# Kernel optimization log

Measured on AMD Instinct MI355X. Metric: run time of the kernel, lower is better.

The kernel has to match this reference:

```python
import jax, jax.numpy as jnp
import numpy as np

DIM = 768
NUM_HEADS = 12
HEAD_DIM = DIM // NUM_HEADS
SCALE = HEAD_DIM ** -0.5
B, N = 8, 1024


def setup_inputs() -> dict:
    key = jax.random.key(0)
    k1, k2, k3, k4, k5 = jax.random.split(key, 5)
    x = jax.random.normal(k1, (B, N, DIM), dtype=jnp.float32)
    # qkv: Linear(dim, 3*dim, bias=False); proj: Linear(dim, dim) with bias
    w_qkv = jax.random.normal(k2, (3 * DIM, DIM), dtype=jnp.float32) * (DIM ** -0.5)
    w_proj = jax.random.normal(k3, (DIM, DIM), dtype=jnp.float32) * (DIM ** -0.5)
    b_proj = jnp.zeros((DIM,), dtype=jnp.float32)
    # learned attention mask parameter, shape (H, L, L) with L >= N
    att_mask = jax.random.normal(k4, (NUM_HEADS, N, N), dtype=jnp.float32)
    return {"x": x, "w_qkv": w_qkv, "w_proj": w_proj, "b_proj": b_proj, "att_mask": att_mask}


def reference(x, w_qkv, w_proj, b_proj, att_mask):
    Bx, Nx, C = x.shape
    # qkv projection -> (3, B, H, N, head_dim)
    qkv = (x @ w_qkv.T).reshape(Bx, Nx, 3, NUM_HEADS, C // NUM_HEADS)
    qkv = jnp.transpose(qkv, (2, 0, 3, 1, 4))
    q, k, v = qkv[0], qkv[1], qkv[2]  # gpd_ratio==active_ratio==1 -> scaling factor 1
    # scores [B, H, N, N]
    attn = jnp.einsum('bhnd,bhmd->bhnm', q, k) * SCALE
    # custom sigmoid mask gating before softmax (broadcast over batch)
    attn = attn * jax.nn.sigmoid(att_mask[:, :Nx, :Nx])[None, :, :, :]
    attn = jax.nn.softmax(attn, axis=-1)
    out = jnp.einsum('bhnm,bhmd->bhnd', attn, v)
    out = jnp.transpose(out, (0, 2, 1, 3)).reshape(Bx, Nx, C)
    return out @ w_proj.T + b_proj
```

## Files before the change

kernel.cpp:

```cpp
#include <hip/hip_runtime.h>
#include <math.h>
#include <stdint.h>

typedef unsigned short u16;
typedef __attribute__((ext_vector_type(8))) short short8;
typedef __attribute__((ext_vector_type(4))) float f32x4;

#define GATE_SCALE 0.18033688011112042f

#if __has_builtin(__builtin_amdgcn_exp2f)
#define FEXP2(x) __builtin_amdgcn_exp2f(x)
#else
#define FEXP2(x) exp2f(x)
#endif

__device__ __forceinline__ u16 f2b(float f) {
    union { float f; unsigned u; } v; v.f = f;
    unsigned r = v.u + 0x7fffu + ((v.u >> 16) & 1u);
    return (u16)(r >> 16);
}
__device__ __forceinline__ u16 f2b_hu(float f) {
    union { float f; unsigned u; } v; v.f = f;
    return (u16)((v.u + 0x8000u) >> 16);
}
__device__ __forceinline__ float b2f(u16 u) {
    union { float f; unsigned u; } v; v.u = ((unsigned)u) << 16; return v.f;
}

#define GLL16(gsrc, ldsbase) __builtin_amdgcn_global_load_lds(                    \
    (__attribute__((address_space(1))) void*)(uintptr_t)(gsrc),                   \
    (__attribute__((address_space(3))) void*)(uint32_t)(uintptr_t)(ldsbase),      \
    16, 0, 0)

#define NX4  1572864
#define NW14 442368
#define NW24 147456
#define NXW4 (NX4 + NW14 + NW24)

__global__ __launch_bounds__(256) void prep_xw(
    const float4* __restrict__ x, const float4* __restrict__ wq,
    const float4* __restrict__ wp,
    ushort4* __restrict__ xb, ushort4* __restrict__ wqb,
    ushort4* __restrict__ wpb)
{
    size_t i = (size_t)blockIdx.x * 256 + threadIdx.x;
    float4 v; ushort4* dst; size_t j;
    if (i < NX4)            { j = i;               v = x[j];  dst = xb;  }
    else if (i < NX4 + NW14){ j = i - NX4;         v = wq[j]; dst = wqb; }
    else                    { j = i - (NX4 + NW14);v = wp[j]; dst = wpb; }
    ushort4 o; o.x = f2b(v.x); o.y = f2b(v.y); o.z = f2b(v.z); o.w = f2b(v.w);
    dst[j] = o;
}

__global__ __launch_bounds__(256) void prep_gate(
    const float4* __restrict__ mask4, u16* __restrict__ gp)
{
    __shared__ u16 L[64][72];
    const int bid = blockIdx.x;
    const int kt = bid & 15, qt = (bid >> 4) & 15, h = bid >> 8;
    const int t = threadIdx.x;

    #pragma unroll
    for (int s = 0; s < 4; ++s) {
        const int idx = t + s * 256;
        const int row = idx >> 4, c4 = idx & 15;
        float4 v = mask4[(size_t)(h * 1024 + qt * 64 + row) * 256 + kt * 16 + c4];
        L[row][c4 * 4 + 0] = f2b(GATE_SCALE / (1.f + __expf(-v.x)));
        L[row][c4 * 4 + 1] = f2b(GATE_SCALE / (1.f + __expf(-v.y)));
        L[row][c4 * 4 + 2] = f2b(GATE_SCALE / (1.f + __expf(-v.z)));
        L[row][c4 * 4 + 3] = f2b(GATE_SCALE / (1.f + __expf(-v.w)));
    }
    __syncthreads();

    const int w = t >> 6, l = t & 63;
    const int fq = l >> 4, fr = l & 15;
    union { u16 u[16]; float4 f[2]; } vals;
    #pragma unroll
    for (int i = 0; i < 4; ++i)
        #pragma unroll
        for (int nt = 0; nt < 4; ++nt)
            vals.u[i * 4 + nt] = L[16 * w + 4 * fq + i][nt * 16 + fr];
    float4* dst = (float4*)(gp + (size_t)bid * 4096 + (size_t)t * 16);
    dst[0] = vals.f[0];
    dst[1] = vals.f[1];
}

__global__ __launch_bounds__(256) void qkv_gemm(
    const u16* __restrict__ xb, const u16* __restrict__ wb,
    u16* __restrict__ qb, u16* __restrict__ kb, u16* __restrict__ vb)
{
    __shared__ u16 As[2][4096];
    __shared__ u16 Bs[2][4096];
    const int t = threadIdx.x, l = t & 63, w = t >> 6;
    const int wm = (w & 1) * 64, wn = (w >> 1) * 64;
    const int m0 = blockIdx.y * 128, c0 = blockIdx.x * 128;

    f32x4 acc[4][4];
    #pragma unroll
    for (int i = 0; i < 4; ++i)
        #pragma unroll
        for (int j = 0; j < 4; ++j) { f32x4 z = {0.f,0.f,0.f,0.f}; acc[i][j] = z; }

    const int srow = l >> 2, sseg = l & 3;
    const int gcol = ((sseg ^ (srow & 3)) << 3);
    const u16* a0 = xb + (size_t)(m0 + w * 16 + srow) * 768 + gcol;
    const u16* a1 = a0 + (size_t)64 * 768;
    const u16* b0p = wb + (size_t)(c0 + w * 16 + srow) * 768 + gcol;
    const u16* b1p = b0p + (size_t)64 * 768;
    const int wofs = w * 512;

    const int fr = l & 15, fq = l >> 4;
    const int fseg = (fq ^ (fr & 3)) << 3;

    GLL16(a0, &As[0][wofs]);
    GLL16(a1, &As[0][2048 + wofs]);
    GLL16(b0p, &Bs[0][wofs]);
    GLL16(b1p, &Bs[0][2048 + wofs]);

    for (int kt = 0; kt < 24; ++kt) {
        __syncthreads();
        if (kt < 23) {
            const int kn = (kt + 1) * 32;
            const int nb = (kt + 1) & 1;
            GLL16(a0 + kn, &As[nb][wofs]);
            GLL16(a1 + kn, &As[nb][2048 + wofs]);
            GLL16(b0p + kn, &Bs[nb][wofs]);
            GLL16(b1p + kn, &Bs[nb][2048 + wofs]);
        }
        const u16* A = As[kt & 1];
        const u16* B = Bs[kt & 1];
        short8 af[4], bf[4];
        #pragma unroll
        for (int mt = 0; mt < 4; ++mt)
            af[mt] = *(const short8*)&A[(wm + mt * 16 + fr) * 32 + fseg];
        #pragma unroll
        for (int nt = 0; nt < 4; ++nt)
            bf[nt] = *(const short8*)&B[(wn + nt * 16 + fr) * 32 + fseg];
        #pragma unroll
        for (int mt = 0; mt < 4; ++mt)
            #pragma unroll
            for (int nt = 0; nt < 4; ++nt)
                acc[mt][nt] = __builtin_amdgcn_mfma_f32_16x16x32_bf16(
                    af[mt], bf[nt], acc[mt][nt], 0, 0, 0);
    }

    const int b = m0 >> 10;
    const int n0 = m0 & 1023;
    #pragma unroll
    for (int nt = 0; nt < 4; ++nt) {
        const int c = c0 + wn + nt * 16 + fr;
        const int which = c / 768;
        const int rem = c - which * 768;
        const int h = rem >> 6, d = rem & 63;
        if (which < 2) {
            u16* dst = ((which == 0) ? qb : kb)
                       + ((size_t)(b * 12 + h) * 1024) * 64 + d;
            #pragma unroll
            for (int mt = 0; mt < 4; ++mt)
                #pragma unroll
                for (int r = 0; r < 4; ++r) {
                    const int n = n0 + wm + mt * 16 + fq * 4 + r;
                    dst[(size_t)n * 64] = f2b(acc[mt][nt][r]);
                }
        } else {
            u16* dst = vb + ((size_t)(b * 12 + h) * 64 + d) * 1024
                          + n0 + wm + fq * 4;
            #pragma unroll
            for (int mt = 0; mt < 4; ++mt) {
                ushort4 pk;
                pk.x = f2b(acc[mt][nt][0]); pk.y = f2b(acc[mt][nt][1]);
                pk.z = f2b(acc[mt][nt][2]); pk.w = f2b(acc[mt][nt][3]);
                *(ushort4*)(dst + mt * 16) = pk;
            }
        }
    }
}

__global__ __launch_bounds__(256, 3) void flash_attn(
    const u16* __restrict__ qb, const u16* __restrict__ kb,
    const u16* __restrict__ vt, const u16* __restrict__ gperm,
    u16* __restrict__ aob)
{
    __shared__ u16 Qs[8192], Ks[4096], Vts[4096], Ps[4096];
    const int t = threadIdx.x, l = t & 63, w = t >> 6;
    const int bid = blockIdx.x;
    const int qtb = bid & 7, bh = bid >> 3;
    const int h = bh % 12, b = bh / 12;
    const int q0 = qtb * 128;

    const u16* hq = qb + (size_t)bh * 65536;
    const u16* hk = kb + (size_t)bh * 65536;
    const u16* hv = vt + (size_t)bh * 65536;
    const u16* hgb = gperm + ((size_t)h * 256 + qtb * 32) * 4096 + (w * 64 + l) * 16;

    const int sr = l >> 3, ss = l & 7;
    const int sg = ((ss ^ (sr & 7)) << 3);
    const int j0 = w * 2, j1 = j0 + 1;

    #pragma unroll
    for (int jq = 0; jq < 4; ++jq) {
        const int j = w * 4 + jq;
        GLL16(hq + (size_t)(q0 + j * 8 + sr) * 64 + sg, Qs + j * 512);
    }
    GLL16(hk + (size_t)(j0 * 8 + sr) * 64 + sg, Ks + j0 * 512);
    GLL16(hk + (size_t)(j1 * 8 + sr) * 64 + sg, Ks + j1 * 512);
    GLL16(hv + (size_t)(j0 * 8 + sr) * 1024 + sg, Vts + j0 * 512);
    GLL16(hv + (size_t)(j1 * 8 + sr) * 1024 + sg, Vts + j1 * 512);
    __syncthreads();

    const int fq = l >> 4, fr = l & 15;
    const int sega = ((fq ^ (fr & 7)) << 3);
    const int segb = (((4 + fq) ^ (fr & 7)) << 3);

    short8 aq[2][2];
    #pragma unroll
    for (int qh = 0; qh < 2; ++qh) {
        const int row = 16 * w + fr;
        aq[qh][0] = *(const short8*)&Qs[qh * 4096 + row * 64 + sega];
        aq[qh][1] = *(const short8*)&Qs[qh * 4096 + row * 64 + segb];
    }

    short8 gn[4];
    gn[0] = *(const short8*)(hgb);
    gn[1] = *(const short8*)(hgb + 8);
    gn[2] = *(const short8*)(hgb + 65536);
    gn[3] = *(const short8*)(hgb + 65536 + 8);

    float l_part[2][4] = {{0.f,0.f,0.f,0.f},{0.f,0.f,0.f,0.f}};
    f32x4 o[2][4];
    #pragma unroll
    for (int qh = 0; qh < 2; ++qh)
        #pragma unroll
        for (int nt = 0; nt < 4; ++nt) { f32x4 z = {0.f,0.f,0.f,0.f}; o[qh][nt] = z; }

    for (int kt = 0; kt < 16; ++kt) {
        short8 g[4];
        #pragma unroll
        for (int s = 0; s < 4; ++s) g[s] = gn[s];
        if (kt < 15) {
            const size_t go = (size_t)(kt + 1) * 4096;
            gn[0] = *(const short8*)(hgb + go);
            gn[1] = *(const short8*)(hgb + go + 8);
            gn[2] = *(const short8*)(hgb + 65536 + go);
            gn[3] = *(const short8*)(hgb + 65536 + go + 8);
        }

        f32x4 sv[2][4];
        #pragma unroll
        for (int nt = 0; nt < 4; ++nt) {
            short8 kf0 = *(const short8*)&Ks[(nt * 16 + fr) * 64 + sega];
            short8 kf1 = *(const short8*)&Ks[(nt * 16 + fr) * 64 + segb];
            f32x4 z0 = {0.f,0.f,0.f,0.f};
            z0 = __builtin_amdgcn_mfma_f32_16x16x32_bf16(aq[0][0], kf0, z0, 0, 0, 0);
            z0 = __builtin_amdgcn_mfma_f32_16x16x32_bf16(aq[0][1], kf1, z0, 0, 0, 0);
            sv[0][nt] = z0;
            f32x4 z1 = {0.f,0.f,0.f,0.f};
            z1 = __builtin_amdgcn_mfma_f32_16x16x32_bf16(aq[1][0], kf0, z1, 0, 0, 0);
            z1 = __builtin_amdgcn_mfma_f32_16x16x32_bf16(aq[1][1], kf1, z1, 0, 0, 0);
            sv[1][nt] = z1;
        }

        short8 ap[2][2];
        #pragma unroll
        for (int qh = 0; qh < 2; ++qh) {
            #pragma unroll
            for (int i = 0; i < 4; ++i) {
                const int pr = 4 * fq + i;
                #pragma unroll
                for (int nt = 0; nt < 4; ++nt) {
                    const int idx = i * 4 + nt;
                    const float gv = b2f((u16)(idx < 8 ? g[2 * qh][idx]
                                                       : g[2 * qh + 1][idx - 8]));
                    const float p = FEXP2(sv[qh][nt][i] * gv);
                    l_part[qh][i] += p;
                    const int col = nt * 16 + fr;
                    Ps[w * 1024 + pr * 64 + (((col >> 3) ^ (pr & 7)) << 3) + (col & 7)]
                        = f2b_hu(p);
                }
            }
            ap[qh][0] = *(const short8*)&Ps[w * 1024 + fr * 64 + sega];
            ap[qh][1] = *(const short8*)&Ps[w * 1024 + fr * 64 + segb];
        }

        #pragma unroll
        for (int nt = 0; nt < 4; ++nt) {
            short8 vf0 = *(const short8*)&Vts[(nt * 16 + fr) * 64 + sega];
            short8 vf1 = *(const short8*)&Vts[(nt * 16 + fr) * 64 + segb];
            o[0][nt] = __builtin_amdgcn_mfma_f32_16x16x32_bf16(ap[0][0], vf0, o[0][nt], 0, 0, 0);
            o[0][nt] = __builtin_amdgcn_mfma_f32_16x16x32_bf16(ap[0][1], vf1, o[0][nt], 0, 0, 0);
            o[1][nt] = __builtin_amdgcn_mfma_f32_16x16x32_bf16(ap[1][0], vf0, o[1][nt], 0, 0, 0);
            o[1][nt] = __builtin_amdgcn_mfma_f32_16x16x32_bf16(ap[1][1], vf1, o[1][nt], 0, 0, 0);
        }

        if (kt < 15) {
            __syncthreads();
            const size_t ko = (size_t)(kt + 1) * 64;
            GLL16(hk + (ko + j0 * 8 + sr) * 64 + sg, Ks + j0 * 512);
            GLL16(hk + (ko + j1 * 8 + sr) * 64 + sg, Ks + j1 * 512);
            GLL16(hv + (size_t)(j0 * 8 + sr) * 1024 + ko + sg, Vts + j0 * 512);
            GLL16(hv + (size_t)(j1 * 8 + sr) * 1024 + ko + sg, Vts + j1 * 512);
            __syncthreads();
        }
    }

    #pragma unroll
    for (int qh = 0; qh < 2; ++qh) {
        #pragma unroll
        for (int i = 0; i < 4; ++i) {
            float s = l_part[qh][i];
            s += __shfl_xor(s, 1, 16);
            s += __shfl_xor(s, 2, 16);
            s += __shfl_xor(s, 4, 16);
            s += __shfl_xor(s, 8, 16);
            const float inv = 1.f / s;
            const int n = q0 + qh * 64 + 16 * w + 4 * fq + i;
            const size_t rowoff = ((size_t)b * 1024 + n) * 768 + h * 64;
            #pragma unroll
            for (int nt = 0; nt < 4; ++nt)
                aob[rowoff + nt * 16 + fr] = f2b(o[qh][nt][i] * inv);
        }
    }
}

__global__ __launch_bounds__(256) void proj_gemm(
    const u16* __restrict__ aob, const u16* __restrict__ wb,
    const float* __restrict__ bproj, float* __restrict__ out)
{
    __shared__ u16 As[2][4096];
    __shared__ u16 Bs[2][4096];
    const int t = threadIdx.x, l = t & 63, w = t >> 6;
    const int wm = (w & 1) * 64, wn = (w >> 1) * 64;
    const int m0 = blockIdx.y * 128, c0 = blockIdx.x * 128;

    f32x4 acc[4][4];
    #pragma unroll
    for (int i = 0; i < 4; ++i)
        #pragma unroll
        for (int j = 0; j < 4; ++j) { f32x4 z = {0.f,0.f,0.f,0.f}; acc[i][j] = z; }

    const int srow = l >> 2, sseg = l & 3;
    const int gcol = ((sseg ^ (srow & 3)) << 3);
    const u16* a0 = aob + (size_t)(m0 + w * 16 + srow) * 768 + gcol;
    const u16* a1 = a0 + (size_t)64 * 768;
    const u16* b0p = wb + (size_t)(c0 + w * 16 + srow) * 768 + gcol;
    const u16* b1p = b0p + (size_t)64 * 768;
    const int wofs = w * 512;

    const int fr = l & 15, fq = l >> 4;
    const int fseg = (fq ^ (fr & 3)) << 3;

    GLL16(a0, &As[0][wofs]);
    GLL16(a1, &As[0][2048 + wofs]);
    GLL16(b0p, &Bs[0][wofs]);
    GLL16(b1p, &Bs[0][2048 + wofs]);

    for (int kt = 0; kt < 24; ++kt) {
        __syncthreads();
        if (kt < 23) {
            const int kn = (kt + 1) * 32;
            const int nb = (kt + 1) & 1;
            GLL16(a0 + kn, &As[nb][wofs]);
            GLL16(a1 + kn, &As[nb][2048 + wofs]);
            GLL16(b0p + kn, &Bs[nb][wofs]);
            GLL16(b1p + kn, &Bs[nb][2048 + wofs]);
        }
        const u16* A = As[kt & 1];
        const u16* B = Bs[kt & 1];
        short8 af[4], bf[4];
        #pragma unroll
        for (int mt = 0; mt < 4; ++mt)
            af[mt] = *(const short8*)&A[(wm + mt * 16 + fr) * 32 + fseg];
        #pragma unroll
        for (int nt = 0; nt < 4; ++nt)
            bf[nt] = *(const short8*)&B[(wn + nt * 16 + fr) * 32 + fseg];
        #pragma unroll
        for (int mt = 0; mt < 4; ++mt)
            #pragma unroll
            for (int nt = 0; nt < 4; ++nt)
                acc[mt][nt] = __builtin_amdgcn_mfma_f32_16x16x32_bf16(
                    af[mt], bf[nt], acc[mt][nt], 0, 0, 0);
    }

    #pragma unroll
    for (int nt = 0; nt < 4; ++nt) {
        const int c = c0 + wn + nt * 16 + fr;
        const float bias = bproj[c];
        #pragma unroll
        for (int mt = 0; mt < 4; ++mt)
            #pragma unroll
            for (int r = 0; r < 4; ++r) {
                const int m = m0 + wm + mt * 16 + fq * 4 + r;
                out[(size_t)m * 768 + c] = acc[mt][nt][r] + bias;
            }
    }
}

extern "C" void kernel_launch(void* const* d_in, const int* in_sizes, int n_in,
                              void* d_out, int out_size, void* d_ws, size_t ws_size,
                              hipStream_t stream)
{
    const float* x     = (const float*)d_in[0];
    const float* wqkv  = (const float*)d_in[1];
    const float* wproj = (const float*)d_in[2];
    const float* bproj = (const float*)d_in[3];
    const float* mask  = (const float*)d_in[4];
    float* out = (float*)d_out;

    char* ws = (char*)d_ws;
    u16* gperm  = (u16*)(ws);
    u16* xb     = (u16*)(ws + 25165824);
    u16* wqkvb  = (u16*)(ws + 37748736);
    u16* wprojb = (u16*)(ws + 41287680);
    u16* qb     = (u16*)(ws + 42467328);
    u16* kb     = (u16*)(ws + 55050240);
    u16* vb     = (u16*)(ws + 67633152);
    u16* aob    = (u16*)(ws + 80216064);

    prep_xw<<<NXW4 / 256, 256, 0, stream>>>(
        (const float4*)x, (const float4*)wqkv, (const float4*)wproj,
        (ushort4*)xb, (ushort4*)wqkvb, (ushort4*)wprojb);

    prep_gate<<<3072, 256, 0, stream>>>((const float4*)mask, gperm);

    qkv_gemm<<<dim3(18, 64), 256, 0, stream>>>(xb, wqkvb, qb, kb, vb);

    flash_attn<<<768, 256, 0, stream>>>(qb, kb, vb, gperm, aob);

    proj_gemm<<<dim3(6, 64), 256, 0, stream>>>(aob, wprojb, bproj, out);
}
```

Measured before the change: 246.3 us.

## Triple-buffer GEMM LDS pipeline, remap blocks per XCD, and adjust LDS swizzle

Both QKV and projection GEMMs switch from double to triple-buffered LDS staging with explicit vmcnt waits and a bare s_barrier, so loads run two k-steps ahead. Block indices are remapped so consecutive tiles land on the same XCD (groups of 8) to improve L2 reuse. The XOR swizzle for LDS reads/writes is changed to use (row>>1)&3 to reduce bank conflicts. The cost is more LDS per block, which may lower occupancy.

```diff
diff --git a/kernel.cpp b/kernel.cpp
--- a/kernel.cpp
+++ b/kernel.cpp
@@ -89,11 +89,14 @@
     const u16* __restrict__ xb, const u16* __restrict__ wb,
     u16* __restrict__ qb, u16* __restrict__ kb, u16* __restrict__ vb)
 {
-    __shared__ u16 As[2][4096];
-    __shared__ u16 Bs[2][4096];
+    __shared__ u16 As[3][4096];
+    __shared__ u16 Bs[3][4096];
     const int t = threadIdx.x, l = t & 63, w = t >> 6;
     const int wm = (w & 1) * 64, wn = (w >> 1) * 64;
-    const int m0 = blockIdx.y * 128, c0 = blockIdx.x * 128;
+
+    const int orig = blockIdx.x + 18 * blockIdx.y;
+    const int nid = (orig & 7) * 144 + (orig >> 3);
+    const int m0 = (nid / 18) * 128, c0 = (nid % 18) * 128;
 
     f32x4 acc[4][4];
     #pragma unroll
@@ -102,7 +105,7 @@
         for (int j = 0; j < 4; ++j) { f32x4 z = {0.f,0.f,0.f,0.f}; acc[i][j] = z; }
 
     const int srow = l >> 2, sseg = l & 3;
-    const int gcol = ((sseg ^ (srow & 3)) << 3);
+    const int gcol = ((sseg ^ ((srow >> 1) & 3)) << 3);
     const u16* a0 = xb + (size_t)(m0 + w * 16 + srow) * 768 + gcol;
     const u16* a1 = a0 + (size_t)64 * 768;
     const u16* b0p = wb + (size_t)(c0 + w * 16 + srow) * 768 + gcol;
@@ -110,25 +113,29 @@
     const int wofs = w * 512;
 
     const int fr = l & 15, fq = l >> 4;
-    const int fseg = (fq ^ (fr & 3)) << 3;
-
-    GLL16(a0, &As[0][wofs]);
-    GLL16(a1, &As[0][2048 + wofs]);
-    GLL16(b0p, &Bs[0][wofs]);
-    GLL16(b1p, &Bs[0][2048 + wofs]);
-
+    const int fseg = (fq ^ ((fr >> 1) & 3)) << 3;
+
+    auto stage = [&](int bi, int koff) {
+        GLL16(a0 + koff, &As[bi][wofs]);
+        GLL16(a1 + koff, &As[bi][2048 + wofs]);
+        GLL16(b0p + koff, &Bs[bi][wofs]);
+        GLL16(b1p + koff, &Bs[bi][2048 + wofs]);
+    };
+
+    stage(0, 0);
+    stage(1, 32);
+
+    int cur = 0;
     for (int kt = 0; kt < 24; ++kt) {
-        __syncthreads();
-        if (kt < 23) {
-            const int kn = (kt + 1) * 32;
-            const int nb = (kt + 1) & 1;
-            GLL16(a0 + kn, &As[nb][wofs]);
-            GLL16(a1 + kn, &As[nb][2048 + wofs]);
-            GLL16(b0p + kn, &Bs[nb][wofs]);
-            GLL16(b1p + kn, &Bs[nb][2048 + wofs]);
-        }
-        const u16* A = As[kt & 1];
-        const u16* B = Bs[kt & 1];
+        if (kt < 23) asm volatile("s_waitcnt vmcnt(4)" ::: "memory");
+        else         asm volatile("s_waitcnt vmcnt(0)" ::: "memory");
+        __builtin_amdgcn_s_barrier();
+        if (kt < 22) {
+            const int nn = (cur == 0) ? 2 : cur - 1;
+            stage(nn, (kt + 2) * 32);
+        }
+        const u16* A = As[cur];
+        const u16* B = Bs[cur];
         short8 af[4], bf[4];
         #pragma unroll
         for (int mt = 0; mt < 4; ++mt)
@@ -142,6 +149,7 @@
             for (int nt = 0; nt < 4; ++nt)
                 acc[mt][nt] = __builtin_amdgcn_mfma_f32_16x16x32_bf16(
                     af[mt], bf[nt], acc[mt][nt], 0, 0, 0);
+        cur = (cur == 2) ? 0 : cur + 1;
     }
 
     const int b = m0 >> 10;
@@ -326,11 +334,14 @@
     const u16* __restrict__ aob, const u16* __restrict__ wb,
     const float* __restrict__ bproj, float* __restrict__ out)
 {
-    __shared__ u16 As[2][4096];
-    __shared__ u16 Bs[2][4096];
+    __shared__ u16 As[3][4096];
+    __shared__ u16 Bs[3][4096];
     const int t = threadIdx.x, l = t & 63, w = t >> 6;
     const int wm = (w & 1) * 64, wn = (w >> 1) * 64;
-    const int m0 = blockIdx.y * 128, c0 = blockIdx.x * 128;
+
+    const int orig = blockIdx.x + 6 * blockIdx.y;
+    const int nid = (orig & 7) * 48 + (orig >> 3);
+    const int m0 = (nid / 6) * 128, c0 = (nid % 6) * 128;
 
     f32x4 acc[4][4];
     #pragma unroll
@@ -339,7 +350,7 @@
         for (int j = 0; j < 4; ++j) { f32x4 z = {0.f,0.f,0.f,0.f}; acc[i][j] = z; }
 
     const int srow = l >> 2, sseg = l & 3;
-    const int gcol = ((sseg ^ (srow & 3)) << 3);
+    const int gcol = ((sseg ^ ((srow >> 1) & 3)) << 3);
     const u16* a0 = aob + (size_t)(m0 + w * 16 + srow) * 768 + gcol;
     const u16* a1 = a0 + (size_t)64 * 768;
     const u16* b0p = wb + (size_t)(c0 + w * 16 + srow) * 768 + gcol;
@@ -347,25 +358,29 @@
     const int wofs = w * 512;
 
     const int fr = l & 15, fq = l >> 4;
-    const int fseg = (fq ^ (fr & 3)) << 3;
-
-    GLL16(a0, &As[0][wofs]);
-    GLL16(a1, &As[0][2048 + wofs]);
-    GLL16(b0p, &Bs[0][wofs]);
-    GLL16(b1p, &Bs[0][2048 + wofs]);
-
+    const int fseg = (fq ^ ((fr >> 1) & 3)) << 3;
+
+    auto stage = [&](int bi, int koff) {
+        GLL16(a0 + koff, &As[bi][wofs]);
+        GLL16(a1 + koff, &As[bi][2048 + wofs]);
+        GLL16(b0p + koff, &Bs[bi][wofs]);
+        GLL16(b1p + koff, &Bs[bi][2048 + wofs]);
+    };
+
+    stage(0, 0);
+    stage(1, 32);
+
+    int cur = 0;
     for (int kt = 0; kt < 24; ++kt) {
-        __syncthreads();
-        if (kt < 23) {
-            const int kn = (kt + 1) * 32;
-            const int nb = (kt + 1) & 1;
-            GLL16(a0 + kn, &As[nb][wofs]);
-            GLL16(a1 + kn, &As[nb][2048 + wofs]);
-            GLL16(b0p + kn, &Bs[nb][wofs]);
-            GLL16(b1p + kn, &Bs[nb][2048 + wofs]);
-        }
-        const u16* A = As[kt & 1];
-        const u16* B = Bs[kt & 1];
+        if (kt < 23) asm volatile("s_waitcnt vmcnt(4)" ::: "memory");
+        else         asm volatile("s_waitcnt vmcnt(0)" ::: "memory");
+        __builtin_amdgcn_s_barrier();
+        if (kt < 22) {
+            const int nn = (cur == 0) ? 2 : cur - 1;
+            stage(nn, (kt + 2) * 32);
+        }
+        const u16* A = As[cur];
+        const u16* B = Bs[cur];
         short8 af[4], bf[4];
         #pragma unroll
         for (int mt = 0; mt < 4; ++mt)
@@ -379,6 +394,7 @@
             for (int nt = 0; nt < 4; ++nt)
                 acc[mt][nt] = __builtin_amdgcn_mfma_f32_16x16x32_bf16(
                     af[mt], bf[nt], acc[mt][nt], 0, 0, 0);
+        cur = (cur == 2) ? 0 : cur + 1;
     }
 
     #pragma unroll
```

New measurement: 242.5 us. No clear change (-1.6%).
